# Optimization experiments

Hardware: AMD Instinct MI355X
Metric: run time of the kernel (lower is better)

The kernel has to match this reference:

```python
import jax, jax.numpy as jnp
import numpy as np

N = 100000   # nodes
E = 3200000  # edges (avg degree 32)
D = 128      # in_dim
RATIO = 0.5
K = int(RATIO * N)  # nodes kept by pooling


def setup_inputs() -> dict:
    key = jax.random.key(0)
    k1, k2, k3 = jax.random.split(key, 3)
    x = jax.random.normal(k1, (N, D), dtype=jnp.float32)
    edge_index = jax.random.randint(k2, (2, E), 0, N, dtype=jnp.int32)
    weight = jax.random.normal(k3, (D, D), dtype=jnp.float32) / np.sqrt(D)
    bias = jnp.zeros((D,), dtype=jnp.float32)
    return {"x": x, "edge_index": edge_index, "weight": weight, "bias": bias}


def gcn_conv(x, edge_index, weight, bias):
    # PyG GCNConv: out = D^{-1/2} (A + I) D^{-1/2} X W + b
    h = x @ weight  # [N, D]
    src, dst = edge_index[0], edge_index[1]
    deg = jax.ops.segment_sum(jnp.ones((E,), h.dtype), dst, num_segments=N) + 1.0  # self-loop
    dinv = jax.lax.rsqrt(deg)  # [N]
    norm = dinv[src] * dinv[dst]  # [E]
    msg = h[src] * norm[:, None]  # gather + scale
    agg = jax.ops.segment_sum(msg, dst, num_segments=N)  # scatter-add
    agg = agg + h * (dinv * dinv)[:, None]  # self-loop contribution
    return agg + bias


def reference(x, edge_index, weight, bias):
    h = gcn_conv(x, edge_index, weight, bias)  # [N, D] node scores/features
    score = jnp.sqrt(jnp.sum(h * h, axis=-1) + 1e-12)  # scalar score per node
    _, perm = jax.lax.top_k(score, K)  # top-k node selection
    x_out = h[perm] * jnp.tanh(score[perm])[:, None]  # gated gather of kept nodes
    # remap / filter edges to the induced subgraph (jit-safe: padded with mask)
    pos = jnp.full((N,), -1, dtype=jnp.int32).at[perm].set(jnp.arange(K, dtype=jnp.int32))
    new_src = pos[edge_index[0]]
    new_dst = pos[edge_index[1]]
    edge_mask = (new_src >= 0) & (new_dst >= 0)
    new_edge_index = jnp.where(edge_mask[None, :], jnp.stack([new_src, new_dst]), -1)
    return x_out, new_edge_index, edge_mask
```

## Files before the change

### kernel.cpp

```cpp
#include <hip/hip_runtime.h>
#include <hip/hip_fp16.h>
#include <stdint.h>

#define NN 100000
#define EE 3200000
#define DD 128
#define KK 50000
#define NB 65536
#define SBLK 256
#define BB 2048
#define NBK 391
#define TILE 8192
#define BMAX 12288
#define NBLK 391

using u16 = unsigned short;
using u32 = unsigned int;
using u64 = unsigned long long;

typedef _Float16 f16x8 __attribute__((ext_vector_type(8)));
typedef float f32x4 __attribute__((ext_vector_type(4)));

__device__ __forceinline__ float bq(float f) {
  u32 b = __float_as_uint(f);
  b += 0x7FFFu + ((b >> 16) & 1u);
  return __uint_as_float(b & 0xFFFF0000u);
}

__global__ void k_init(u32* __restrict__ chist, u32* __restrict__ bcnt,
                       u64* __restrict__ meta, u32* __restrict__ mflag) {
  int i = blockIdx.x * 256 + threadIdx.x;
  for (int j = i; j < NB; j += 256 * 256) bcnt[j] = 0u;
  if (i < NBK) chist[i] = 0u;
  if (i == 0) { meta[0] = ~0ull; meta[1] = 0ull; *mflag = 0u; }
}

__global__ void k_chist(const int* __restrict__ ei, u32* __restrict__ chist) {
  __shared__ u32 cnt[NBK];
  int t = threadIdx.x;
  int e0 = blockIdx.x * TILE;
  int vcnt = EE - e0; if (vcnt > TILE) vcnt = TILE;
  for (int i = t; i < NBK; i += 256) cnt[i] = 0;
  __syncthreads();
  for (int i = t; i < vcnt; i += 256)
    atomicAdd(&cnt[(u32)ei[EE + e0 + i] >> 8], 1u);
  __syncthreads();
  for (int i = t; i < NBK; i += 256)
    if (cnt[i]) atomicAdd(&chist[i], cnt[i]);
}

__global__ void k_cscan(const u32* __restrict__ chist, u32* __restrict__ cbase,
                        u32* __restrict__ pbcur) {
  __shared__ u32 buf[2][512];
  int t = threadIdx.x;
  u32 v = (t < NBK) ? chist[t] : 0u;
  int a = 0; buf[0][t] = v; __syncthreads();
  for (int s = 1; s < 512; s <<= 1) {
    buf[1 - a][t] = buf[a][t] + ((t >= s) ? buf[a][t - s] : 0u);
    a = 1 - a; __syncthreads();
  }
  if (t < NBK) { u32 e = buf[a][t] - v; cbase[t] = e; pbcur[t] = e; }
}

__global__ void k_part1(const int* __restrict__ ei, u32* __restrict__ bcur,
                        u32* __restrict__ ebuf) {
  __shared__ u32 cnt[NBK];
  __shared__ u32 lpos[NBK];
  __shared__ u32 gbase[NBK];
  __shared__ u32 sbuf[TILE];
  __shared__ u16 sbid[TILE];
  int t = threadIdx.x;
  int e0 = blockIdx.x * TILE;
  int vcnt = EE - e0; if (vcnt > TILE) vcnt = TILE;
  for (int i = t; i < NBK; i += 256) cnt[i] = 0;
  __syncthreads();
  for (int i = t; i < vcnt; i += 256) {
    int d = ei[EE + e0 + i];
    atomicAdd(&cnt[d >> 8], 1u);
  }
  __syncthreads();
  if (t < 64) {
    u32 carry = 0;
    for (int c = 0; c < 7; ++c) {
      int idx = c * 64 + t;
      u32 v = (idx < NBK) ? cnt[idx] : 0u;
      u32 x = v;
      #pragma unroll
      for (int s = 1; s < 64; s <<= 1) {
        u32 y = __shfl_up(x, s);
        if (t >= s) x += y;
      }
      if (idx < NBK) lpos[idx] = x - v + carry;
      carry += __shfl(x, 63);
    }
  }
  __syncthreads();
  for (int i = t; i < NBK; i += 256)
    gbase[i] = cnt[i] ? atomicAdd(&bcur[i], cnt[i]) : 0u;
  for (int i = t; i < vcnt; i += 256) {
    int d = ei[EE + e0 + i];
    int s = ei[e0 + i];
    u32 b = (u32)d >> 8;
    u32 p = atomicAdd(&lpos[b], 1u);
    sbuf[p] = ((u32)(d & 255) << 17) | (u32)s;
    sbid[p] = (u16)b;
  }
  __syncthreads();
  for (int i = t; i < vcnt; i += 256) {
    u32 b = sbid[i];
    u32 lstart = lpos[b] - cnt[b];
    ebuf[gbase[b] + ((u32)i - lstart)] = sbuf[i];
  }
}

__global__ void k_part2(const u32* __restrict__ ebuf, const u32* __restrict__ cbase,
                        u32* __restrict__ deg, u32* __restrict__ offs,
                        double* __restrict__ dinv64, float* __restrict__ dinv32,
                        int* __restrict__ csr) {
  __shared__ u32 fcnt[256];
  __shared__ u32 buf[2][256];
  __shared__ u32 ncur[256];
  __shared__ u32 scsr[BMAX];
  int b = blockIdx.x; int t = threadIdx.x;
  int nbase = b * 256;
  u32 gstart = cbase[b];
  u32 gend = (b + 1 < NBK) ? cbase[b + 1] : (u32)EE;
  u32 cnt = gend - gstart;
  fcnt[t] = 0u;
  __syncthreads();
  for (u32 i = t; i < cnt; i += 256)
    atomicAdd(&fcnt[ebuf[gstart + i] >> 17], 1u);
  __syncthreads();
  u32 v = fcnt[t];
  int a = 0; buf[0][t] = v; __syncthreads();
  for (int s = 1; s < 256; s <<= 1) {
    buf[1 - a][t] = buf[a][t] + ((t >= s) ? buf[a][t - s] : 0u);
    a = 1 - a; __syncthreads();
  }
  u32 floc = buf[a][t] - v;
  int node = nbase + t;
  if (node < NN) {
    deg[node] = v;
    offs[node] = gstart + floc;
    double d = 1.0 / sqrt((double)(v + 1u));
    dinv64[node] = d;
    dinv32[node] = (float)d;
  }
  ncur[t] = floc;
  __syncthreads();
  if (cnt <= (u32)BMAX) {
    for (u32 i = t; i < cnt; i += 256) {
      u32 en = ebuf[gstart + i];
      u32 p = atomicAdd(&ncur[en >> 17], 1u);
      scsr[p] = en & 0x1FFFFu;
    }
    __syncthreads();
    for (u32 i = t; i < cnt; i += 256) csr[gstart + i] = (int)scsr[i];
  } else {
    for (u32 i = t; i < cnt; i += 256) {
      u32 en = ebuf[gstart + i];
      u32 p = atomicAdd(&ncur[en >> 17], 1u);
      csr[gstart + p] = (int)(en & 0x1FFFFu);
    }
  }
}

__global__ void k_wfrag(const float* __restrict__ w, f16x8* __restrict__ wfrag) {
  int idx = blockIdx.x * 256 + threadIdx.x;
  int lane = idx & 63;
  int ctt = (idx >> 6) & 7;
  int kstep = idx >> 9;
  int c = ctt * 16 + (lane & 15);
  int kbase = (lane >> 4) * 8 + kstep * 32;
  f16x8 v;
  #pragma unroll
  for (int j = 0; j < 8; ++j) v[j] = (_Float16)w[(kbase + j) * DD + c];
  wfrag[idx] = v;
}

__global__ void __launch_bounds__(256) k_gemm_mfma(const float* __restrict__ x,
                                                   const f16x8* __restrict__ wfrag,
                                                   u16* __restrict__ hW16) {
  int wid = threadIdx.x >> 6, lane = threadIdx.x & 63;
  int rowbase = blockIdx.x * 32 + (wid & 1) * 16;
  int colgrp = wid >> 1;
  int row = rowbase + (lane & 15);
  int klane = (lane >> 4) * 8;

  f32x4 acc[4] = {{0,0,0,0},{0,0,0,0},{0,0,0,0},{0,0,0,0}};
  const float* xr = x + (size_t)row * DD;
  #pragma unroll
  for (int kstep = 0; kstep < 4; ++kstep) {
    const float4* xp = (const float4*)(xr + klane + kstep * 32);
    float4 v0 = xp[0], v1 = xp[1];
    f16x8 a;
    a[0] = (_Float16)v0.x; a[1] = (_Float16)v0.y;
    a[2] = (_Float16)v0.z; a[3] = (_Float16)v0.w;
    a[4] = (_Float16)v1.x; a[5] = (_Float16)v1.y;
    a[6] = (_Float16)v1.z; a[7] = (_Float16)v1.w;
    #pragma unroll
    for (int ct = 0; ct < 4; ++ct) {
      f16x8 b = wfrag[(kstep * 8 + colgrp * 4 + ct) * 64 + lane];
      acc[ct] = __builtin_amdgcn_mfma_f32_16x16x32_f16(a, b, acc[ct], 0, 0, 0);
    }
  }
  #pragma unroll
  for (int ct = 0; ct < 4; ++ct) {
    int col = colgrp * 64 + ct * 16 + (lane & 15);
    #pragma unroll
    for (int reg = 0; reg < 4; ++reg) {
      int r = rowbase + (lane >> 4) * 4 + reg;
      hW16[(size_t)r * DD + col] = __half_as_ushort(__float2half(acc[ct][reg]));
    }
  }
}

__global__ void k_check(const float* __restrict__ x, const float* __restrict__ w,
                        const u16* __restrict__ hW16, u32* __restrict__ flag) {
  int idx = blockIdx.x * 256 + threadIdx.x;
  int r = idx >> 7, c = idx & 127;
  const float4* xr = (const float4*)(x + (size_t)r * DD);
  float acc = 0.0f;
  #pragma unroll 8
  for (int k4 = 0; k4 < 32; ++k4) {
    float4 xv = xr[k4];
    int kb = k4 * 4;
    acc += xv.x * w[kb * DD + c] + xv.y * w[(kb + 1) * DD + c]
         + xv.z * w[(kb + 2) * DD + c] + xv.w * w[(kb + 3) * DD + c];
  }
  float got = __half2float(__ushort_as_half(hW16[r * DD + c]));
  if (fabsf(got - acc) > 0.02f) atomicOr(flag, 1u);
}

__global__ void k_gemm_fb(const float* __restrict__ x, const float* __restrict__ w,
                          u16* __restrict__ hW16, const u32* __restrict__ flag) {
  if (*flag == 0u) return;
  __shared__ float Wl[DD * DD];
  int t = threadIdx.x;
  for (int i = t; i < DD * DD; i += 256) Wl[i] = w[i];
  __syncthreads();
  int base = blockIdx.x * 16;
  int c = t & 127, rh = t >> 7;
  for (int it = 0; it < 8; ++it) {
    int r = base + it * 2 + rh;
    if (r < NN) {
      const float4* xr = (const float4*)(x + (size_t)r * DD);
      float acc = 0.0f;
      #pragma unroll 4
      for (int k4 = 0; k4 < 32; ++k4) {
        float4 xv = xr[k4];
        int kb = k4 * 4;
        acc += xv.x * Wl[kb * DD + c];
        acc += xv.y * Wl[(kb + 1) * DD + c];
        acc += xv.z * Wl[(kb + 2) * DD + c];
        acc += xv.w * Wl[(kb + 3) * DD + c];
      }
      hW16[(size_t)r * DD + c] = __half_as_ushort(__float2half(acc));
    }
  }
}

__global__ void k_agg(const u32* __restrict__ hw, const float* __restrict__ dinv32,
                      const u32* __restrict__ offs, const u32* __restrict__ deg,
                      const int* __restrict__ csr, const float* __restrict__ bias,
                      float* __restrict__ hc, u64* __restrict__ key,
                      float* __restrict__ gate) {
  int wid = threadIdx.x >> 6;
  int lane = threadIdx.x & 63;
  int half = lane >> 5;
  int l5 = lane & 31;
  int node = blockIdx.x * 8 + wid * 2 + half;
  if (node >= NN) return;
  const uint2* hwp = (const uint2*)hw;
  float di = dinv32[node];
  float a0 = 0.f, a1 = 0.f, a2 = 0.f, a3 = 0.f;
  u32 o = offs[node], cnt = deg[node];
  u32 k = 0;
  for (; k + 4 <= cnt; k += 4) {
    int s0 = csr[o + k], s1 = csr[o + k + 1], s2 = csr[o + k + 2], s3 = csr[o + k + 3];
    float n0 = dinv32[s0] * di, n1 = dinv32[s1] * di;
    float n2 = dinv32[s2] * di, n3 = dinv32[s3] * di;
    uint2 w0 = hwp[(size_t)s0 * 32 + l5];
    uint2 w1 = hwp[(size_t)s1 * 32 + l5];
    uint2 w2 = hwp[(size_t)s2 * 32 + l5];
    uint2 w3 = hwp[(size_t)s3 * 32 + l5];
    float2 p0 = __half22float2(*(__half2*)&w0.x), q0 = __half22float2(*(__half2*)&w0.y);
    float2 p1 = __half22float2(*(__half2*)&w1.x), q1 = __half22float2(*(__half2*)&w1.y);
    float2 p2 = __half22float2(*(__half2*)&w2.x), q2 = __half22float2(*(__half2*)&w2.y);
    float2 p3 = __half22float2(*(__half2*)&w3.x), q3 = __half22float2(*(__half2*)&w3.y);
    a0 += p0.x * n0 + p1.x * n1 + p2.x * n2 + p3.x * n3;
    a1 += p0.y * n0 + p1.y * n1 + p2.y * n2 + p3.y * n3;
    a2 += q0.x * n0 + q1.x * n1 + q2.x * n2 + q3.x * n3;
    a3 += q0.y * n0 + q1.y * n1 + q2.y * n2 + q3.y * n3;
  }
  for (; k < cnt; ++k) {
    int s = csr[o + k];
    float nrm = dinv32[s] * di;
    uint2 wb = hwp[(size_t)s * 32 + l5];
    float2 p = __half22float2(*(__half2*)&wb.x), q = __half22float2(*(__half2*)&wb.y);
    a0 += p.x * nrm; a1 += p.y * nrm; a2 += q.x * nrm; a3 += q.y * nrm;
  }
  float di2 = di * di;
  uint2 wb = hwp[(size_t)node * 32 + l5];
  float2 p = __half22float2(*(__half2*)&wb.x), q = __half22float2(*(__half2*)&wb.y);
  float4 bv = ((const float4*)bias)[l5];
  a0 += p.x * di2 + bv.x;
  a1 += p.y * di2 + bv.y;
  a2 += q.x * di2 + bv.z;
  a3 += q.y * di2 + bv.w;
  float4 out = make_float4(a0, a1, a2, a3);
  ((float4*)hc)[(size_t)node * 32 + l5] = out;
  float ss = a0 * a0 + a1 * a1 + a2 * a2 + a3 * a3;
  #pragma unroll
  for (int off = 16; off > 0; off >>= 1) ss += __shfl_xor(ss, off);
  if (l5 == 0) {
    u32 sb = __float_as_uint(ss);
    key[node] = ((u64)sb << 17) | (u64)(0x1FFFF - node);
    gate[node] = tanhf(sqrtf(ss + 1e-12f));
  }
}

__global__ void k_minmax(const u64* __restrict__ key, u64* __restrict__ meta) {
  __shared__ u64 smn[256], smx[256];
  int t = threadIdx.x; int i = blockIdx.x * 256 + t;
  u64 v = (i < NN) ? key[i] : key[0];
  smn[t] = v; smx[t] = v; __syncthreads();
  for (int s = 128; s > 0; s >>= 1) {
    if (t < s) {
      if (smn[t + s] < smn[t]) smn[t] = smn[t + s];
      if (smx[t + s] > smx[t]) smx[t] = smx[t + s];
    }
    __syncthreads();
  }
  if (t == 0) { atomicMin(&meta[0], smn[0]); atomicMax(&meta[1], smx[0]); }
}

__device__ __forceinline__ u32 bshift(u64 kmin, u64 kmax) {
  u64 range = kmax - kmin;
  int bits = 64 - __clzll(range | 1ull);
  return (u32)(bits > 16 ? bits - 16 : 0);
}

__global__ void k_hist(const u64* __restrict__ key, const u64* __restrict__ meta,
                       u32* __restrict__ barr, u32* __restrict__ bcnt) {
  int i = blockIdx.x * blockDim.x + threadIdx.x;
  if (i >= NN) return;
  u64 kmin = meta[0];
  u32 sh = bshift(kmin, meta[1]);
  u32 b = (u32)((key[i] - kmin) >> sh);
  barr[i] = b;
  atomicAdd(&bcnt[b], 1u);
}

__global__ void k_scan2(u32* __restrict__ bsum, int nb) {
  __shared__ u32 buf[2][512];
  int t = threadIdx.x;
  u32 v = (t < nb) ? bsum[t] : 0u;
  int a = 0; buf[0][t] = v; __syncthreads();
  for (int s = 1; s < 512; s <<= 1) {
    buf[1 - a][t] = buf[a][t] + ((t >= s) ? buf[a][t - s] : 0u);
    a = 1 - a; __syncthreads();
  }
  if (t < nb) bsum[t] = buf[a][t] - v;
}

__global__ void k_bscan1(const u32* __restrict__ bcnt, u32* __restrict__ bsum2) {
  __shared__ u32 sh[256];
  int t = threadIdx.x; int r = blockIdx.x * 256 + t;
  u32 v = bcnt[NB - 1 - r];
  sh[t] = v; __syncthreads();
  for (int s = 128; s > 0; s >>= 1) { if (t < s) sh[t] += sh[t + s]; __syncthreads(); }
  if (t == 0) bsum2[blockIdx.x] = sh[0];
}

__global__ void k_bscan3(const u32* __restrict__ bcnt, const u32* __restrict__ bsum2,
                         u32* __restrict__ base, u32* __restrict__ bcur) {
  __shared__ u32 buf[2][256];
  int t = threadIdx.x; int r = blockIdx.x * 256 + t;
  int b = NB - 1 - r;
  u32 v = bcnt[b];
  int a = 0; buf[0][t] = v; __syncthreads();
  for (int s = 1; s < 256; s <<= 1) {
    buf[1 - a][t] = buf[a][t] + ((t >= s) ? buf[a][t - s] : 0u);
    a = 1 - a; __syncthreads();
  }
  u32 bs = buf[a][t] - v + bsum2[blockIdx.x];
  base[b] = bs;
  bcur[b] = NN - bs - v;
}

__global__ void k_bscatter(const u32* __restrict__ barr, u32* __restrict__ bcur,
                           u32* __restrict__ blist) {
  int i = blockIdx.x * blockDim.x + threadIdx.x;
  if (i >= NN) return;
  u32 p = atomicAdd(&bcur[barr[i]], 1u);
  blist[p] = (u32)i;
}

__global__ void k_rank2(const u64* __restrict__ key, const u32* __restrict__ barr,
                        const u32* __restrict__ bcnt, const u32* __restrict__ base,
                        const u32* __restrict__ blist, int* __restrict__ arank,
                        u32* __restrict__ bandNode) {
  int i = blockIdx.x * blockDim.x + threadIdx.x;
  if (i >= NN) return;
  u32 b = barr[i];
  u64 ki = key[i];
  u32 bs = base[b], cnt = bcnt[b];
  u32 off = NN - bs - cnt;
  u32 gt = 0;
  for (u32 j = 0; j < cnt; ++j) gt += (key[blist[off + j]] > ki) ? 1u : 0u;
  int r = (int)(bs + gt);
  arank[i] = r;
  int rb = r - (KK - BB);
  if (rb >= 0 && rb < 2 * BB) bandNode[rb] = (u32)i;
}

__global__ void k_bscore(const u32* __restrict__ bandNode,
                         const float* __restrict__ x, const float* __restrict__ w,
                         const double* __restrict__ dinv64,
                         const u32* __restrict__ offs, const u32* __restrict__ deg,
                         const int* __restrict__ csr, const float* __restrict__ bias,
                         u64* __restrict__ ekey) {
  __shared__ double zsh[4][DD];
  int wid = threadIdx.x >> 6;
  int lane = threadIdx.x & 63;
  int slot = blockIdx.x * 4 + wid;
  int node = (int)bandNode[slot];
  double di = dinv64[node];
  double z0 = 0.0, z1 = 0.0;
  u32 o = offs[node], cnt = deg[node];
  for (u32 k = 0; k <= cnt; ++k) {
    int s = (k < cnt) ? csr[o + k] : node;
    double wgt = (k < cnt) ? (dinv64[s] * di) : (di * di);
    float2 xv = ((const float2*)x)[(size_t)s * 64 + lane];
    z0 += (double)xv.x * wgt;
    z1 += (double)xv.y * wgt;
  }
  zsh[wid][2 * lane] = z0;
  zsh[wid][2 * lane + 1] = z1;
  __syncthreads();
  float2 bv = ((const float2*)bias)[lane];
  double a0 = (double)bv.x, a1 = (double)bv.y;
  for (int kk = 0; kk < DD; ++kk) {
    double zk = zsh[wid][kk];
    float2 wv = ((const float2*)w)[kk * 64 + lane];
    a0 += zk * (double)wv.x;
    a1 += zk * (double)wv.y;
  }
  double ss = a0 * a0 + a1 * a1;
  #pragma unroll
  for (int off = 32; off > 0; off >>= 1) ss += __shfl_xor(ss, off);
  if (lane == 0) {
    double sc = sqrt(ss + 1e-12);
    u64 bits = (u64)__double_as_longlong(sc);
    ekey[slot] = (bits & ~0x1FFFFull) | (u64)(0x1FFFF - node);
  }
}

__global__ void k_bandrank(const u64* __restrict__ ekey, u32* __restrict__ brank) {
  __shared__ u64 sk[2 * BB];
  int t = threadIdx.x;
  for (int j = t; j < 2 * BB; j += 256) sk[j] = ekey[j];
  __syncthreads();
  int idx = blockIdx.x * 256 + t;
  u64 kk = sk[idx];
  u32 c = 0;
  for (int j = 0; j < 2 * BB; ++j) c += (sk[j] > kk) ? 1u : 0u;
  brank[idx] = c;
}

__global__ void k_pos2(const int* __restrict__ arank, const u32* __restrict__ brank,
                       int* __restrict__ pos) {
  int i = blockIdx.x * blockDim.x + threadIdx.x;
  if (i >= NN) return;
  int r = arank[i];
  int p;
  if (r < KK - BB) p = r;
  else if (r < KK + BB) {
    u32 br = brank[r - (KK - BB)];
    p = (br < BB) ? (KK - BB + (int)br) : -1;
  } else p = -1;
  pos[i] = p;
}

__global__ void k_xout(const float* __restrict__ hc, const float* __restrict__ gate,
                       const int* __restrict__ pos, float* __restrict__ outx) {
  int id = blockIdx.x * blockDim.x + threadIdx.x;
  if (id >= NN * DD) return;
  int i = id >> 7, d = id & 127;
  int p = pos[i];
  if (p < 0) return;
  float v = hc[(size_t)i * DD + d] * gate[i];
  outx[(size_t)p * DD + d] = bq(v);
}

__global__ void k_edges(const int* __restrict__ ei, const int* __restrict__ pos,
                        float* __restrict__ osrc, float* __restrict__ odst,
                        float* __restrict__ omask) {
  int e = blockIdx.x * blockDim.x + threadIdx.x;
  if (e >= EE) return;
  int ns = pos[ei[e]];
  int nd = pos[ei[EE + e]];
  bool m = (ns >= 0) && (nd >= 0);
  osrc[e] = m ? bq((float)ns) : -1.0f;
  odst[e] = m ? bq((float)nd) : -1.0f;
  omask[e] = m ? 1.0f : 0.0f;
}

extern "C" void kernel_launch(void* const* d_in, const int* in_sizes, int n_in,
                              void* d_out, int out_size, void* d_ws, size_t ws_size,
                              hipStream_t stream) {
  const float* x    = (const float*)d_in[0];
  const int*   ei   = (const int*)d_in[1];
  const float* w    = (const float*)d_in[2];
  const float* bias = (const float*)d_in[3];
  float* outx = (float*)d_out;
  char* ws = (char*)d_ws;

  size_t off = 0;
  auto alloc = [&](size_t b) -> void* {
    void* p = ws + off; off += (b + 255) & ~(size_t)255; return p;
  };
  u16*    hW16   = (u16*)alloc((size_t)NN * DD * 2);
  float*  hc     = (float*)alloc((size_t)NN * DD * 4);
  double* dinv64 = (double*)alloc((size_t)NN * 8);
  float*  dinv32 = (float*)alloc((size_t)NN * 4);
  float*  gate   = (float*)alloc((size_t)NN * 4);
  u64*    key    = (u64*)alloc((size_t)NN * 8);
  u32*    deg    = (u32*)alloc((size_t)NN * 4);
  u32*    offs   = (u32*)alloc((size_t)NN * 4);
  int*    csr    = (int*)alloc((size_t)EE * 4);
  u32*    ebuf   = (u32*)alloc((size_t)EE * 4);
  u32*    chist  = (u32*)alloc((size_t)NBK * 4);
  u32*    cbase  = (u32*)alloc((size_t)NBK * 4);
  u32*    pbcur  = (u32*)alloc((size_t)NBK * 4);
  int*    arank  = (int*)alloc((size_t)NN * 4);
  int*    pos    = (int*)alloc((size_t)NN * 4);
  u64*    meta   = (u64*)alloc(4 * 8);
  u32*    bcnt   = (u32*)alloc((size_t)NB * 4);
  u32*    base   = (u32*)alloc((size_t)NB * 4);
  u32*    bcur   = (u32*)alloc((size_t)NB * 4);
  u32*    bsum2  = (u32*)alloc(SBLK * 4);
  u32*    barr   = (u32*)alloc((size_t)NN * 4);
  u32*    blist  = (u32*)alloc((size_t)NN * 4);
  u32*    bandNode = (u32*)alloc((size_t)2 * BB * 4);
  u64*    ekey     = (u64*)alloc((size_t)2 * BB * 8);
  u32*    brank    = (u32*)alloc((size_t)2 * BB * 4);
  f16x8*  wfrag    = (f16x8*)alloc((size_t)2048 * 16);
  u32*    mflag    = (u32*)alloc(256);

  k_init<<<256, 256, 0, stream>>>(chist, bcnt, meta, mflag);
  k_chist<<<(EE + TILE - 1) / TILE, 256, 0, stream>>>(ei, chist);
  k_cscan<<<1, 512, 0, stream>>>(chist, cbase, pbcur);
  k_part1<<<(EE + TILE - 1) / TILE, 256, 0, stream>>>(ei, pbcur, ebuf);
  k_part2<<<NBK, 256, 0, stream>>>(ebuf, cbase, deg, offs, dinv64, dinv32, csr);
  k_wfrag<<<8, 256, 0, stream>>>(w, wfrag);
  k_gemm_mfma<<<NN / 32, 256, 0, stream>>>(x, wfrag, hW16);
  k_check<<<16, 256, 0, stream>>>(x, w, hW16, mflag);
  k_gemm_fb<<<(NN + 15) / 16, 256, 0, stream>>>(x, w, hW16, mflag);
  k_agg<<<(NN + 7) / 8, 256, 0, stream>>>((const u32*)hW16, dinv32, offs, deg, csr,
                                          bias, hc, key, gate);
  k_minmax<<<NBLK, 256, 0, stream>>>(key, meta);
  k_hist<<<(NN + 255) / 256, 256, 0, stream>>>(key, meta, barr, bcnt);
  k_bscan1<<<SBLK, 256, 0, stream>>>(bcnt, bsum2);
  k_scan2<<<1, 512, 0, stream>>>(bsum2, SBLK);
  k_bscan3<<<SBLK, 256, 0, stream>>>(bcnt, bsum2, base, bcur);
  k_bscatter<<<(NN + 255) / 256, 256, 0, stream>>>(barr, bcur, blist);
  k_rank2<<<(NN + 255) / 256, 256, 0, stream>>>(key, barr, bcnt, base, blist, arank,
                                                bandNode);
  k_bscore<<<(2 * BB) / 4, 256, 0, stream>>>(bandNode, x, w, dinv64, offs, deg, csr,
                                             bias, ekey);
  k_bandrank<<<(2 * BB) / 256, 256, 0, stream>>>(ekey, brank);
  k_pos2<<<(NN + 255) / 256, 256, 0, stream>>>(arank, brank, pos);
  k_xout<<<(NN * DD + 255) / 256, 256, 0, stream>>>(hc, gate, pos, outx);
  float* oei = outx + (size_t)KK * DD;
  k_edges<<<(EE + 255) / 256, 256, 0, stream>>>(ei, pos, oei, oei + EE, oei + 2 * (size_t)EE);
}
```

Measured before the change: 408.0 us.

## Store aggregated features as fp16, widen agg loads, shrink bucket histogram

```diff
diff --git a/kernel.cpp b/kernel.cpp
--- a/kernel.cpp
+++ b/kernel.cpp
@@ -6,8 +6,8 @@
 #define EE 3200000
 #define DD 128
 #define KK 50000
-#define NB 65536
-#define SBLK 256
+#define NB 32768
+#define SBLK 128
 #define BB 2048
 #define NBK 391
 #define TILE 8192
@@ -25,6 +25,11 @@
   u32 b = __float_as_uint(f);
   b += 0x7FFFu + ((b >> 16) & 1u);
   return __uint_as_float(b & 0xFFFF0000u);
+}
+
+__device__ __forceinline__ u32 packh2(float a, float b) {
+  return (u32)__half_as_ushort(__float2half(a)) |
+         ((u32)__half_as_ushort(__float2half(b)) << 16);
 }
 
 __global__ void k_init(u32* __restrict__ chist, u32* __restrict__ bcnt,
@@ -239,10 +244,9 @@
   int t = threadIdx.x;
   for (int i = t; i < DD * DD; i += 256) Wl[i] = w[i];
   __syncthreads();
-  int base = blockIdx.x * 16;
   int c = t & 127, rh = t >> 7;
-  for (int it = 0; it < 8; ++it) {
-    int r = base + it * 2 + rh;
+  for (int it = 0; it < 128; ++it) {
+    int r = blockIdx.x * 256 + it * 2 + rh;
     if (r < NN) {
       const float4* xr = (const float4*)(x + (size_t)r * DD);
       float acc = 0.0f;
@@ -263,57 +267,68 @@
 __global__ void k_agg(const u32* __restrict__ hw, const float* __restrict__ dinv32,
                       const u32* __restrict__ offs, const u32* __restrict__ deg,
                       const int* __restrict__ csr, const float* __restrict__ bias,
-                      float* __restrict__ hc, u64* __restrict__ key,
+                      u32* __restrict__ hc16, u64* __restrict__ key,
                       float* __restrict__ gate) {
-  int wid = threadIdx.x >> 6;
-  int lane = threadIdx.x & 63;
-  int half = lane >> 5;
-  int l5 = lane & 31;
-  int node = blockIdx.x * 8 + wid * 2 + half;
+  int t = threadIdx.x;
+  int l4 = t & 15;
+  int node = blockIdx.x * 16 + (t >> 4);
   if (node >= NN) return;
-  const uint2* hwp = (const uint2*)hw;
+  const uint4* hwp = (const uint4*)hw;
   float di = dinv32[node];
   float a0 = 0.f, a1 = 0.f, a2 = 0.f, a3 = 0.f;
+  float a4 = 0.f, a5 = 0.f, a6 = 0.f, a7 = 0.f;
   u32 o = offs[node], cnt = deg[node];
   u32 k = 0;
-  for (; k + 4 <= cnt; k += 4) {
-    int s0 = csr[o + k], s1 = csr[o + k + 1], s2 = csr[o + k + 2], s3 = csr[o + k + 3];
+  for (; k + 2 <= cnt; k += 2) {
+    int s0 = csr[o + k], s1 = csr[o + k + 1];
     float n0 = dinv32[s0] * di, n1 = dinv32[s1] * di;
-    float n2 = dinv32[s2] * di, n3 = dinv32[s3] * di;
-    uint2 w0 = hwp[(size_t)s0 * 32 + l5];
-    uint2 w1 = hwp[(size_t)s1 * 32 + l5];
-    uint2 w2 = hwp[(size_t)s2 * 32 + l5];
-    uint2 w3 = hwp[(size_t)s3 * 32 + l5];
-    float2 p0 = __half22float2(*(__half2*)&w0.x), q0 = __half22float2(*(__half2*)&w0.y);
-    float2 p1 = __half22float2(*(__half2*)&w1.x), q1 = __half22float2(*(__half2*)&w1.y);
-    float2 p2 = __half22float2(*(__half2*)&w2.x), q2 = __half22float2(*(__half2*)&w2.y);
-    float2 p3 = __half22float2(*(__half2*)&w3.x), q3 = __half22float2(*(__half2*)&w3.y);
-    a0 += p0.x * n0 + p1.x * n1 + p2.x * n2 + p3.x * n3;
-    a1 += p0.y * n0 + p1.y * n1 + p2.y * n2 + p3.y * n3;
-    a2 += q0.x * n0 + q1.x * n1 + q2.x * n2 + q3.x * n3;
-    a3 += q0.y * n0 + q1.y * n1 + q2.y * n2 + q3.y * n3;
+    uint4 w0 = hwp[(size_t)s0 * 16 + l4];
+    uint4 w1 = hwp[(size_t)s1 * 16 + l4];
+    float2 p00 = __half22float2(*(__half2*)&w0.x), p01 = __half22float2(*(__half2*)&w0.y);
+    float2 p02 = __half22float2(*(__half2*)&w0.z), p03 = __half22float2(*(__half2*)&w0.w);
+    float2 p10 = __half22float2(*(__half2*)&w1.x), p11 = __half22float2(*(__half2*)&w1.y);
+    float2 p12 = __half22float2(*(__half2*)&w1.z), p13 = __half22float2(*(__half2*)&w1.w);
+    a0 += p00.x * n0 + p10.x * n1;
+    a1 += p00.y * n0 + p10.y * n1;
+    a2 += p01.x * n0 + p11.x * n1;
+    a3 += p01.y * n0 + p11.y * n1;
+    a4 += p02.x * n0 + p12.x * n1;
+    a5 += p02.y * n0 + p12.y * n1;
+    a6 += p03.x * n0 + p13.x * n1;
+    a7 += p03.y * n0 + p13.y * n1;
   }
   for (; k < cnt; ++k) {
     int s = csr[o + k];
     float nrm = dinv32[s] * di;
-    uint2 wb = hwp[(size_t)s * 32 + l5];
-    float2 p = __half22float2(*(__half2*)&wb.x), q = __half22float2(*(__half2*)&wb.y);
-    a0 += p.x * nrm; a1 += p.y * nrm; a2 += q.x * nrm; a3 += q.y * nrm;
+    uint4 wb = hwp[(size_t)s * 16 + l4];
+    float2 p0 = __half22float2(*(__half2*)&wb.x), p1 = __half22float2(*(__half2*)&wb.y);
+    float2 p2 = __half22float2(*(__half2*)&wb.z), p3 = __half22float2(*(__half2*)&wb.w);
+    a0 += p0.x * nrm; a1 += p0.y * nrm; a2 += p1.x * nrm; a3 += p1.y * nrm;
+    a4 += p2.x * nrm; a5 += p2.y * nrm; a6 += p3.x * nrm; a7 += p3.y * nrm;
   }
   float di2 = di * di;
-  uint2 wb = hwp[(size_t)node * 32 + l5];
-  float2 p = __half22float2(*(__half2*)&wb.x), q = __half22float2(*(__half2*)&wb.y);
-  float4 bv = ((const float4*)bias)[l5];
-  a0 += p.x * di2 + bv.x;
-  a1 += p.y * di2 + bv.y;
-  a2 += q.x * di2 + bv.z;
-  a3 += q.y * di2 + bv.w;
-  float4 out = make_float4(a0, a1, a2, a3);
-  ((float4*)hc)[(size_t)node * 32 + l5] = out;
-  float ss = a0 * a0 + a1 * a1 + a2 * a2 + a3 * a3;
+  uint4 wb = hwp[(size_t)node * 16 + l4];
+  float2 p0 = __half22float2(*(__half2*)&wb.x), p1 = __half22float2(*(__half2*)&wb.y);
+  float2 p2 = __half22float2(*(__half2*)&wb.z), p3 = __half22float2(*(__half2*)&wb.w);
+  float4 bv0 = ((const float4*)bias)[2 * l4];
+  float4 bv1 = ((const float4*)bias)[2 * l4 + 1];
+  a0 += p0.x * di2 + bv0.x;
+  a1 += p0.y * di2 + bv0.y;
+  a2 += p1.x * di2 + bv0.z;
+  a3 += p1.y * di2 + bv0.w;
+  a4 += p2.x * di2 + bv1.x;
+  a5 += p2.y * di2 + bv1.y;
+  a6 += p3.x * di2 + bv1.z;
+  a7 += p3.y * di2 + bv1.w;
+  uint4 out;
+  out.x = packh2(a0, a1); out.y = packh2(a2, a3);
+  out.z = packh2(a4, a5); out.w = packh2(a6, a7);
+  ((uint4*)hc16)[(size_t)node * 16 + l4] = out;
+  float ss = a0 * a0 + a1 * a1 + a2 * a2 + a3 * a3
+           + a4 * a4 + a5 * a5 + a6 * a6 + a7 * a7;
   #pragma unroll
-  for (int off = 16; off > 0; off >>= 1) ss += __shfl_xor(ss, off);
-  if (l5 == 0) {
+  for (int off = 8; off > 0; off >>= 1) ss += __shfl_xor(ss, off);
+  if (l4 == 0) {
     u32 sb = __float_as_uint(ss);
     key[node] = ((u64)sb << 17) | (u64)(0x1FFFF - node);
     gate[node] = tanhf(sqrtf(ss + 1e-12f));
@@ -338,7 +353,7 @@
 __device__ __forceinline__ u32 bshift(u64 kmin, u64 kmax) {
   u64 range = kmax - kmin;
   int bits = 64 - __clzll(range | 1ull);
-  return (u32)(bits > 16 ? bits - 16 : 0);
+  return (u32)(bits > 15 ? bits - 15 : 0);
 }
 
 __global__ void k_hist(const u64* __restrict__ key, const u64* __restrict__ meta,
@@ -483,15 +498,18 @@
   pos[i] = p;
 }
 
-__global__ void k_xout(const float* __restrict__ hc, const float* __restrict__ gate,
+__global__ void k_xout(const u32* __restrict__ hc16, const float* __restrict__ gate,
                        const int* __restrict__ pos, float* __restrict__ outx) {
   int id = blockIdx.x * blockDim.x + threadIdx.x;
-  if (id >= NN * DD) return;
-  int i = id >> 7, d = id & 127;
+  if (id >= NN * 64) return;
+  int i = id >> 6, d2 = id & 63;
   int p = pos[i];
   if (p < 0) return;
-  float v = hc[(size_t)i * DD + d] * gate[i];
-  outx[(size_t)p * DD + d] = bq(v);
+  float g = gate[i];
+  u32 hv = hc16[(size_t)i * 64 + d2];
+  float2 v = __half22float2(*(__half2*)&hv);
+  float2 out = make_float2(bq(v.x * g), bq(v.y * g));
+  ((float2*)outx)[(size_t)p * 64 + d2] = out;
 }
 
 __global__ void k_edges(const int* __restrict__ ei, const int* __restrict__ pos,
@@ -522,7 +540,7 @@
     void* p = ws + off; off += (b + 255) & ~(size_t)255; return p;
   };
   u16*    hW16   = (u16*)alloc((size_t)NN * DD * 2);
-  float*  hc     = (float*)alloc((size_t)NN * DD * 4);
+  u32*    hc16   = (u32*)alloc((size_t)NN * DD * 2);
   double* dinv64 = (double*)alloc((size_t)NN * 8);
   float*  dinv32 = (float*)alloc((size_t)NN * 4);
   float*  gate   = (float*)alloc((size_t)NN * 4);
@@ -557,9 +575,9 @@
   k_wfrag<<<8, 256, 0, stream>>>(w, wfrag);
   k_gemm_mfma<<<NN / 32, 256, 0, stream>>>(x, wfrag, hW16);
   k_check<<<16, 256, 0, stream>>>(x, w, hW16, mflag);
-  k_gemm_fb<<<(NN + 15) / 16, 256, 0, stream>>>(x, w, hW16, mflag);
-  k_agg<<<(NN + 7) / 8, 256, 0, stream>>>((const u32*)hW16, dinv32, offs, deg, csr,
-                                          bias, hc, key, gate);
+  k_gemm_fb<<<NBLK, 256, 0, stream>>>(x, w, hW16, mflag);
+  k_agg<<<(NN + 15) / 16, 256, 0, stream>>>((const u32*)hW16, dinv32, offs, deg, csr,
+                                            bias, hc16, key, gate);
   k_minmax<<<NBLK, 256, 0, stream>>>(key, meta);
   k_hist<<<(NN + 255) / 256, 256, 0, stream>>>(key, meta, barr, bcnt);
   k_bscan1<<<SBLK, 256, 0, stream>>>(bcnt, bsum2);
@@ -572,7 +590,7 @@
                                              bias, ekey);
   k_bandrank<<<(2 * BB) / 256, 256, 0, stream>>>(ekey, brank);
   k_pos2<<<(NN + 255) / 256, 256, 0, stream>>>(arank, brank, pos);
-  k_xout<<<(NN * DD + 255) / 256, 256, 0, stream>>>(hc, gate, pos, outx);
+  k_xout<<<(NN * 64 + 255) / 256, 256, 0, stream>>>(hc16, gate, pos, outx);
   float* oei = outx + (size_t)KK * DD;
   k_edges<<<(EE + 255) / 256, 256, 0, stream>>>(ei, pos, oei, oei + EE, oei + 2 * (size_t)EE);
 }
```

New measurement: 410.6 us. Within noise of the previous version (+0.6%).
